# Kernel optimization log

Hardware: AMD Instinct MI355X
Metric: run time of the kernel (lower is better)

The kernel has to match this reference:

```python
import jax, jax.numpy as jnp
import numpy as np

B, S = 4096, 8192

def setup_inputs() -> dict:
    key = jax.random.key(0)
    c = jax.random.normal(key, (B, S), dtype=jnp.float32)
    beta = jnp.asarray(10.0, dtype=jnp.float32)
    return {"c": c, "beta": beta}

def reference(c, beta):
    # Original per-step recurrence:
    #   delta_i = (1/beta) * logsumexp([beta*delta_{i-1}, beta*(c_i + delta_{i-1})])
    #           = delta_{i-1} + (1/beta) * log(1 + exp(beta * c_i))
    # i.e. an exact prefix sum of softplus(beta*c)/beta along S.
    # (Note: the torch code stacks delta_prev, not 0, as the first branch,
    #  so the logsumexp telescopes to a cumulative sum.)
    step = jax.nn.softplus(beta * c) / beta          # (B, S)
    return jnp.cumsum(step, axis=1)                  # (B, S) propagated delays
```

## Files before the change

### kernel.cpp

```cpp
#include <hip/hip_runtime.h>
#include <hip/hip_bf16.h>


#define ROW_S 8192
#define BLOCK_T 256

__device__ __forceinline__ int swz(int f) { return f ^ ((f >> 3) & 7); }

__device__ __forceinline__ float softplus_step(float c, float beta, float inv_beta) {
    float tb = beta * c;
    float a  = fabsf(tb);
    float e  = __expf(-a);
    float l  = __logf(1.0f + e);
    return (fmaxf(tb, 0.0f) + l) * inv_beta;
}

__global__ __launch_bounds__(BLOCK_T) void softplus_cumsum_kernel(
    const float* __restrict__ c,
    const float* __restrict__ beta_p,
    float* __restrict__ out)
{
    __shared__ float4 lds[ROW_S / 4];
    __shared__ float  wave_sums[BLOCK_T / 64];

    const int t    = threadIdx.x;
    const int lane = t & 63;
    const int wave = t >> 6;
    const size_t row_base = (size_t)blockIdx.x * ROW_S;

    const float beta     = beta_p[0];
    const float inv_beta = 1.0f / beta;

    const float4* in4  = (const float4*)(c + row_base);
    float4*       out4 = (float4*)(out + row_base);

    #pragma unroll
    for (int j = 0; j < 8; ++j) {
        int f = j * BLOCK_T + t;
        float4 v = in4[f];
        float4 s;
        s.x = softplus_step(v.x, beta, inv_beta);
        s.y = softplus_step(v.y, beta, inv_beta);
        s.z = softplus_step(v.z, beta, inv_beta);
        s.w = softplus_step(v.w, beta, inv_beta);
        lds[swz(f)] = s;
    }
    __syncthreads();

    float r[32];
    float run = 0.0f;
    #pragma unroll
    for (int k = 0; k < 8; ++k) {
        int f = t * 8 + k;
        float4 v = lds[swz(f)];
        run += v.x; r[4 * k + 0] = run;
        run += v.y; r[4 * k + 1] = run;
        run += v.z; r[4 * k + 2] = run;
        run += v.w; r[4 * k + 3] = run;
    }
    const float total = run;

    float x = total;
    #pragma unroll
    for (int d = 1; d < 64; d <<= 1) {
        float y = __shfl_up(x, d, 64);
        if (lane >= d) x += y;
    }
    if (lane == 63) wave_sums[wave] = x;
    __syncthreads();

    float off = x - total;
    #pragma unroll
    for (int w = 0; w < BLOCK_T / 64; ++w)
        if (w < wave) off += wave_sums[w];

    #pragma unroll
    for (int k = 0; k < 8; ++k) {
        int f = t * 8 + k;
        float4 s;
        s.x = r[4 * k + 0] + off;
        s.y = r[4 * k + 1] + off;
        s.z = r[4 * k + 2] + off;
        s.w = r[4 * k + 3] + off;
        lds[swz(f)] = s;
    }
    __syncthreads();

    #pragma unroll
    for (int j = 0; j < 8; ++j) {
        int f = j * BLOCK_T + t;
        out4[f] = lds[swz(f)];
    }
}

extern "C" void kernel_launch(void* const* d_in, const int* in_sizes, int n_in,
                              void* d_out, int out_size, void* d_ws, size_t ws_size,
                              hipStream_t stream) {
    const float* c      = (const float*)d_in[0];
    const float* beta_p = (const float*)d_in[1];
    float*       out    = (float*)d_out;

    const int B = in_sizes[0] / ROW_S;
    softplus_cumsum_kernel<<<dim3(B), dim3(BLOCK_T), 0, stream>>>(c, beta_p, out);
}
```

Measured before the change: 233.4 us.

## Replace LDS row transpose with per-chunk wave scans in registers

Drops the 32 KB shared-memory staging buffer and its transpose. Each thread now keeps its coalesced float4 chunks in registers and runs a wave shuffle scan for each of the 8 chunks, and a small shared array of wave sums supplies the carry between chunks. This removes two LDS round trips and two barriers and frees LDS for higher occupancy. In exchange it performs eight times as many shuffle scans.

```diff
diff --git a/kernel.cpp b/kernel.cpp
--- a/kernel.cpp
+++ b/kernel.cpp
@@ -2,10 +2,10 @@
 #include <hip/hip_bf16.h>
 
 
-#define ROW_S 8192
+#define ROW_S   8192
 #define BLOCK_T 256
-
-__device__ __forceinline__ int swz(int f) { return f ^ ((f >> 3) & 7); }
+#define NJ      (ROW_S / 4 / BLOCK_T)
+#define NWAVE   (BLOCK_T / 64)
 
 __device__ __forceinline__ float softplus_step(float c, float beta, float inv_beta) {
     float tb = beta * c;
@@ -20,8 +20,7 @@
     const float* __restrict__ beta_p,
     float* __restrict__ out)
 {
-    __shared__ float4 lds[ROW_S / 4];
-    __shared__ float  wave_sums[BLOCK_T / 64];
+    __shared__ float wave_sums[NJ][NWAVE];
 
     const int t    = threadIdx.x;
     const int lane = t & 63;
@@ -31,65 +30,62 @@
     const float beta     = beta_p[0];
     const float inv_beta = 1.0f / beta;
 
-    const float4* in4  = (const float4*)(c + row_base);
-    float4*       out4 = (float4*)(out + row_base);
+    const float4* __restrict__ in4  = (const float4*)(c + row_base);
+    float4*       __restrict__ out4 = (float4*)(out + row_base);
 
+    float4 v[NJ];
     #pragma unroll
-    for (int j = 0; j < 8; ++j) {
-        int f = j * BLOCK_T + t;
-        float4 v = in4[f];
-        float4 s;
-        s.x = softplus_step(v.x, beta, inv_beta);
-        s.y = softplus_step(v.y, beta, inv_beta);
-        s.z = softplus_step(v.z, beta, inv_beta);
-        s.w = softplus_step(v.w, beta, inv_beta);
-        lds[swz(f)] = s;
+    for (int j = 0; j < NJ; ++j)
+        v[j] = in4[j * BLOCK_T + t];
+
+    float4 r[NJ];
+    float  s[NJ];
+    #pragma unroll
+    for (int j = 0; j < NJ; ++j) {
+        float a = softplus_step(v[j].x, beta, inv_beta);
+        float b = softplus_step(v[j].y, beta, inv_beta);
+        float d = softplus_step(v[j].z, beta, inv_beta);
+        float e = softplus_step(v[j].w, beta, inv_beta);
+        r[j].x = a;
+        r[j].y = a + b;
+        r[j].z = r[j].y + d;
+        r[j].w = r[j].z + e;
+        s[j]   = r[j].w;
+    }
+
+    float xscan[NJ];
+    #pragma unroll
+    for (int j = 0; j < NJ; ++j) {
+        float x = s[j];
+        #pragma unroll
+        for (int d = 1; d < 64; d <<= 1) {
+            float y = __shfl_up(x, d, 64);
+            if (lane >= d) x += y;
+        }
+        xscan[j] = x;
+        if (lane == 63) wave_sums[j][wave] = x;
     }
     __syncthreads();
 
-    float r[32];
-    float run = 0.0f;
+    float carry = 0.0f;
     #pragma unroll
-    for (int k = 0; k < 8; ++k) {
-        int f = t * 8 + k;
-        float4 v = lds[swz(f)];
-        run += v.x; r[4 * k + 0] = run;
-        run += v.y; r[4 * k + 1] = run;
-        run += v.z; r[4 * k + 2] = run;
-        run += v.w; r[4 * k + 3] = run;
-    }
-    const float total = run;
+    for (int j = 0; j < NJ; ++j) {
+        float woff = 0.0f, btot = 0.0f;
+        #pragma unroll
+        for (int w = 0; w < NWAVE; ++w) {
+            float ws = wave_sums[j][w];
+            if (w < wave) woff += ws;
+            btot += ws;
+        }
+        const float off = carry + woff + (xscan[j] - s[j]);
+        carry += btot;
 
-    float x = total;
-    #pragma unroll
-    for (int d = 1; d < 64; d <<= 1) {
-        float y = __shfl_up(x, d, 64);
-        if (lane >= d) x += y;
-    }
-    if (lane == 63) wave_sums[wave] = x;
-    __syncthreads();
-
-    float off = x - total;
-    #pragma unroll
-    for (int w = 0; w < BLOCK_T / 64; ++w)
-        if (w < wave) off += wave_sums[w];
-
-    #pragma unroll
-    for (int k = 0; k < 8; ++k) {
-        int f = t * 8 + k;
-        float4 s;
-        s.x = r[4 * k + 0] + off;
-        s.y = r[4 * k + 1] + off;
-        s.z = r[4 * k + 2] + off;
-        s.w = r[4 * k + 3] + off;
-        lds[swz(f)] = s;
-    }
-    __syncthreads();
-
-    #pragma unroll
-    for (int j = 0; j < 8; ++j) {
-        int f = j * BLOCK_T + t;
-        out4[f] = lds[swz(f)];
+        float4 o;
+        o.x = r[j].x + off;
+        o.y = r[j].y + off;
+        o.z = r[j].z + off;
+        o.w = r[j].w + off;
+        out4[j * BLOCK_T + t] = o;
     }
 }
 
```

Result: no change. 233.1 us (-0.2%).
